# Kernel tuning notes

Measured on AMD Instinct MI355X. Metric: run time of the kernel, lower is better.

Reference implementation:

```python
import jax, jax.numpy as jnp
import numpy as np

B, T, I, H, L, O = 2048, 512, 1, 64, 2, 1


def _lstm_layer(x, Wih, Whh, b):
    """Single LSTM layer, batch_first x: [B, T, in] -> [B, T, H].
    PyTorch gate order: i, f, g, o. b = b_ih + b_hh (folded)."""
    Bn = x.shape[0]
    Hn = Whh.shape[1]
    # Precompute input contribution for all timesteps (hoisted out of scan)
    xg = jnp.einsum('bti,gi->btg', x, Wih) + b  # [B, T, 4H]

    def step(carry, xg_t):
        h, c = carry
        g = xg_t + h @ Whh.T  # [B, 4H]
        i, f, gg, o = jnp.split(g, 4, axis=-1)
        i = jax.nn.sigmoid(i)
        f = jax.nn.sigmoid(f)
        gg = jnp.tanh(gg)
        o = jax.nn.sigmoid(o)
        c = f * c + i * gg
        h = o * jnp.tanh(c)
        return (h, c), h

    h0 = jnp.zeros((Bn, Hn), x.dtype)
    c0 = jnp.zeros((Bn, Hn), x.dtype)
    (_, _), hs = jax.lax.scan(step, (h0, c0), jnp.swapaxes(xg, 0, 1))  # hs: [T, B, H]
    return jnp.swapaxes(hs, 0, 1)


def setup_inputs() -> dict:
    key = jax.random.key(0)
    ks = jax.random.split(key, 11)
    s = 1.0 / np.sqrt(H)  # torch default uniform bound
    u = lambda k, shp: jax.random.uniform(k, shp, jnp.float32, -s, s)
    return {
        'x': jax.random.normal(ks[0], (B, T, I), jnp.float32),
        'Wih0': u(ks[1], (4 * H, I)),
        'Whh0': u(ks[2], (4 * H, H)),
        'bih0': u(ks[3], (4 * H,)),
        'bhh0': u(ks[4], (4 * H,)),
        'Wih1': u(ks[5], (4 * H, H)),
        'Whh1': u(ks[6], (4 * H, H)),
        'bih1': u(ks[7], (4 * H,)),
        'bhh1': u(ks[8], (4 * H,)),
        'fcW': u(ks[9], (O, H)),
        'fcb': u(ks[10], (O,)),
    }


def reference(x, Wih0, Whh0, bih0, bhh0, Wih1, Whh1, bih1, bhh1, fcW, fcb):
    h1 = _lstm_layer(x, Wih0, Whh0, bih0 + bhh0)   # [B, T, H]
    h2 = _lstm_layer(h1, Wih1, Whh1, bih1 + bhh1)  # [B, T, H]
    return h2[:, -1, :] @ fcW.T + fcb               # [B, O]
```

## Files before the change

### kernel.cpp

```cpp
#include <hip/hip_runtime.h>


#define TT 512
#define HH 64
#define BT 8

typedef __attribute__((ext_vector_type(8))) short short8;
typedef __attribute__((ext_vector_type(4))) float f32x4;

#define MFMA16 __builtin_amdgcn_mfma_f32_16x16x32_bf16

__device__ __forceinline__ float sigm(float x) {
    return __builtin_amdgcn_rcpf(1.f + __expf(-x));
}
__device__ __forceinline__ float tanh_f(float x) {
    return 1.f - 2.f * __builtin_amdgcn_rcpf(1.f + __expf(2.f * x));
}
__device__ __forceinline__ void cvt8(const float* p, short8& hi, short8& lo) {
    #pragma unroll
    for (int i = 0; i < 8; ++i) {
        float v = p[i];
        unsigned short h = (unsigned short)(__float_as_uint(v) >> 16);
        float r = v - __uint_as_float(((unsigned)h) << 16);
        unsigned short l = (unsigned short)(__float_as_uint(r) >> 16);
        hi[i] = (short)h;
        lo[i] = (short)l;
    }
}
__device__ __forceinline__ void split1(float v, unsigned short& h, unsigned short& l) {
    h = (unsigned short)(__float_as_uint(v) >> 16);
    float r = v - __uint_as_float(((unsigned)h) << 16);
    l = (unsigned short)(__float_as_uint(r) >> 16);
}
__device__ __forceinline__ float gate4(float pi, float pf, float pg, float po, float& c) {
    float gi = sigm(pi), gf = sigm(pf), gg = tanh_f(pg), go = sigm(po);
    c = fmaf(gf, c, gi * gg);
    return go * tanh_f(c);
}
__device__ __forceinline__ float dpp_ror8(float v) {
    return __int_as_float(__builtin_amdgcn_update_dpp(
        0, __float_as_int(v), 0x128, 0xF, 0xF, true));
}

__global__ __launch_bounds__(1024) void lstm_mfma(
    const float* __restrict__ x,
    const float* __restrict__ Wih0, const float* __restrict__ Whh0,
    const float* __restrict__ bih0, const float* __restrict__ bhh0,
    const float* __restrict__ Wih1, const float* __restrict__ Whh1,
    const float* __restrict__ bih1, const float* __restrict__ bhh1,
    const float* __restrict__ fcW, const float* __restrict__ fcb,
    float* __restrict__ out)
{
    __shared__ float xs[BT][TT + 1];
    __shared__ __align__(16) short aH1[2][2][2][64][8];
    __shared__ __align__(16) short aH2[2][2][2][64][8];
    __shared__ float hF[BT][HH + 1];
    __shared__ float fcw_s[HH];

    const int t    = threadIdx.x;
    const int lane = t & 63;
    const int w    = t >> 6;
    const bool isL1 = (w < 8);
    const int wv   = w & 7;
    const int b0   = blockIdx.x * BT;
    const int m    = lane & 15;
    const int q    = lane >> 4;

    for (int i = t; i < BT * TT; i += 1024)
        xs[i >> 9][i & (TT - 1)] = x[(size_t)(b0 + (i >> 9)) * TT + (i & (TT - 1))];
    {
        int* z1 = (int*)aH1;
        for (int i = t; i < 2048; i += 1024) z1[i] = 0;
        int* z2 = (int*)aH2;
        for (int i = t; i < 2048; i += 1024) z2[i] = 0;
    }
    if (t < HH) fcw_s[t] = fcW[t];

    short8 aWh[2][4], aWl[2][4];
    {
        const float* Ws01 = isL1 ? Whh0 : Wih1;
        #pragma unroll
        for (int i = 0; i < 2; ++i) {
            const int mtg = 2 * wv + i;
            const int rho = (m & 3) * 64 + 4 * mtg + (m >> 2);
            cvt8(Ws01 + rho * HH +      q * 8, aWh[i][0], aWl[i][0]);
            cvt8(Ws01 + rho * HH + 32 + q * 8, aWh[i][1], aWl[i][1]);
            if (!isL1) {
                cvt8(Whh1 + rho * HH +      q * 8, aWh[i][2], aWl[i][2]);
                cvt8(Whh1 + rho * HH + 32 + q * 8, aWh[i][3], aWl[i][3]);
            }
        }
    }

    f32x4 biasD[2];
    #pragma unroll
    for (int i = 0; i < 2; ++i)
        #pragma unroll
        for (int r = 0; r < 4; ++r) {
            const int rho = r * 64 + 4 * (2 * wv + i) + q;
            biasD[i][r] = isL1 ? (bih0[rho] + bhh0[rho])
                               : (bih1[rho] + bhh1[rho]);
        }

    const int ts  = (m >> 3) & 1;
    const int jpk = 8 * wv + 4 * ts + q;
    const int bpk = m & 7;
    float wxb[4];
    #pragma unroll
    for (int v = 0; v < 4; ++v)
        wxb[v] = isL1 ? Wih0[v * 64 + jpk] : 0.f;
    const int skt = jpk >> 5;
    const int ssl = bpk + 16 * ((jpk >> 3) & 3);
    const int sse = jpk & 7;
    float c = 0.f;

    __syncthreads();

    #pragma unroll 2
    for (int k = 0; k < TT; ++k) {
        const int p = k & 1, pn = p ^ 1;

        if (isL1) {
            short8 bh0 = *(const short8*)&aH1[p][0][0][lane][0];
            short8 bl0 = *(const short8*)&aH1[p][0][1][lane][0];
            short8 bh1 = *(const short8*)&aH1[p][1][0][lane][0];
            short8 bl1 = *(const short8*)&aH1[p][1][1][lane][0];
            f32x4 acc0 = biasD[0], acc1 = biasD[1];
            acc0 = MFMA16(aWh[0][0], bh0, acc0, 0, 0, 0);
            acc1 = MFMA16(aWh[1][0], bh0, acc1, 0, 0, 0);
            acc0 = MFMA16(aWl[0][0], bh0, acc0, 0, 0, 0);
            acc1 = MFMA16(aWl[1][0], bh0, acc1, 0, 0, 0);
            acc0 = MFMA16(aWh[0][0], bl0, acc0, 0, 0, 0);
            acc1 = MFMA16(aWh[1][0], bl0, acc1, 0, 0, 0);
            acc0 = MFMA16(aWh[0][1], bh1, acc0, 0, 0, 0);
            acc1 = MFMA16(aWh[1][1], bh1, acc1, 0, 0, 0);
            acc0 = MFMA16(aWl[0][1], bh1, acc0, 0, 0, 0);
            acc1 = MFMA16(aWl[1][1], bh1, acc1, 0, 0, 0);
            acc0 = MFMA16(aWh[0][1], bl1, acc0, 0, 0, 0);
            acc1 = MFMA16(aWh[1][1], bl1, acc1, 0, 0, 0);
            f32x4 mv, pk;
            #pragma unroll
            for (int r = 0; r < 4; ++r) mv[r] = dpp_ror8(acc1[r]);
            #pragma unroll
            for (int r = 0; r < 4; ++r) pk[r] = (m < 8) ? acc0[r] : mv[r];
            float xb = xs[bpk][k];
            float h1 = gate4(fmaf(wxb[0], xb, pk[0]),
                             fmaf(wxb[1], xb, pk[1]),
                             fmaf(wxb[2], xb, pk[2]),
                             fmaf(wxb[3], xb, pk[3]), c);
            unsigned short hh, hl;
            split1(h1, hh, hl);
            aH1[pn][skt][0][ssl][sse] = (short)hh;
            aH1[pn][skt][1][ssl][sse] = (short)hl;
        } else if (k > 0) {
            short8 b1h0 = *(const short8*)&aH1[p][0][0][lane][0];
            short8 b1l0 = *(const short8*)&aH1[p][0][1][lane][0];
            short8 b1h1 = *(const short8*)&aH1[p][1][0][lane][0];
            short8 b1l1 = *(const short8*)&aH1[p][1][1][lane][0];
            short8 b2h0 = *(const short8*)&aH2[p][0][0][lane][0];
            short8 b2l0 = *(const short8*)&aH2[p][0][1][lane][0];
            short8 b2h1 = *(const short8*)&aH2[p][1][0][lane][0];
            short8 b2l1 = *(const short8*)&aH2[p][1][1][lane][0];
            f32x4 acc0 = biasD[0], acc1 = biasD[1];
            acc0 = MFMA16(aWh[0][0], b1h0, acc0, 0, 0, 0);
            acc1 = MFMA16(aWh[1][0], b1h0, acc1, 0, 0, 0);
            acc0 = MFMA16(aWl[0][0], b1h0, acc0, 0, 0, 0);
            acc1 = MFMA16(aWl[1][0], b1h0, acc1, 0, 0, 0);
            acc0 = MFMA16(aWh[0][0], b1l0, acc0, 0, 0, 0);
            acc1 = MFMA16(aWh[1][0], b1l0, acc1, 0, 0, 0);
            acc0 = MFMA16(aWh[0][1], b1h1, acc0, 0, 0, 0);
            acc1 = MFMA16(aWh[1][1], b1h1, acc1, 0, 0, 0);
            acc0 = MFMA16(aWl[0][1], b1h1, acc0, 0, 0, 0);
            acc1 = MFMA16(aWl[1][1], b1h1, acc1, 0, 0, 0);
            acc0 = MFMA16(aWh[0][1], b1l1, acc0, 0, 0, 0);
            acc1 = MFMA16(aWh[1][1], b1l1, acc1, 0, 0, 0);
            acc0 = MFMA16(aWh[0][2], b2h0, acc0, 0, 0, 0);
            acc1 = MFMA16(aWh[1][2], b2h0, acc1, 0, 0, 0);
            acc0 = MFMA16(aWl[0][2], b2h0, acc0, 0, 0, 0);
            acc1 = MFMA16(aWl[1][2], b2h0, acc1, 0, 0, 0);
            acc0 = MFMA16(aWh[0][2], b2l0, acc0, 0, 0, 0);
            acc1 = MFMA16(aWh[1][2], b2l0, acc1, 0, 0, 0);
            acc0 = MFMA16(aWh[0][3], b2h1, acc0, 0, 0, 0);
            acc1 = MFMA16(aWh[1][3], b2h1, acc1, 0, 0, 0);
            acc0 = MFMA16(aWl[0][3], b2h1, acc0, 0, 0, 0);
            acc1 = MFMA16(aWl[1][3], b2h1, acc1, 0, 0, 0);
            acc0 = MFMA16(aWh[0][3], b2l1, acc0, 0, 0, 0);
            acc1 = MFMA16(aWh[1][3], b2l1, acc1, 0, 0, 0);
            f32x4 mv, pk;
            #pragma unroll
            for (int r = 0; r < 4; ++r) mv[r] = dpp_ror8(acc1[r]);
            #pragma unroll
            for (int r = 0; r < 4; ++r) pk[r] = (m < 8) ? acc0[r] : mv[r];
            float h2 = gate4(pk[0], pk[1], pk[2], pk[3], c);
            unsigned short hh, hl;
            split1(h2, hh, hl);
            aH2[pn][skt][0][ssl][sse] = (short)hh;
            aH2[pn][skt][1][ssl][sse] = (short)hl;
        }
        __syncthreads();
    }

    if (!isL1) {
        short8 b1h0 = *(const short8*)&aH1[0][0][0][lane][0];
        short8 b1l0 = *(const short8*)&aH1[0][0][1][lane][0];
        short8 b1h1 = *(const short8*)&aH1[0][1][0][lane][0];
        short8 b1l1 = *(const short8*)&aH1[0][1][1][lane][0];
        short8 b2h0 = *(const short8*)&aH2[0][0][0][lane][0];
        short8 b2l0 = *(const short8*)&aH2[0][0][1][lane][0];
        short8 b2h1 = *(const short8*)&aH2[0][1][0][lane][0];
        short8 b2l1 = *(const short8*)&aH2[0][1][1][lane][0];
        f32x4 acc0 = biasD[0], acc1 = biasD[1];
        acc0 = MFMA16(aWh[0][0], b1h0, acc0, 0, 0, 0);
        acc1 = MFMA16(aWh[1][0], b1h0, acc1, 0, 0, 0);
        acc0 = MFMA16(aWl[0][0], b1h0, acc0, 0, 0, 0);
        acc1 = MFMA16(aWl[1][0], b1h0, acc1, 0, 0, 0);
        acc0 = MFMA16(aWh[0][0], b1l0, acc0, 0, 0, 0);
        acc1 = MFMA16(aWh[1][0], b1l0, acc1, 0, 0, 0);
        acc0 = MFMA16(aWh[0][1], b1h1, acc0, 0, 0, 0);
        acc1 = MFMA16(aWh[1][1], b1h1, acc1, 0, 0, 0);
        acc0 = MFMA16(aWl[0][1], b1h1, acc0, 0, 0, 0);
        acc1 = MFMA16(aWl[1][1], b1h1, acc1, 0, 0, 0);
        acc0 = MFMA16(aWh[0][1], b1l1, acc0, 0, 0, 0);
        acc1 = MFMA16(aWh[1][1], b1l1, acc1, 0, 0, 0);
        acc0 = MFMA16(aWh[0][2], b2h0, acc0, 0, 0, 0);
        acc1 = MFMA16(aWh[1][2], b2h0, acc1, 0, 0, 0);
        acc0 = MFMA16(aWl[0][2], b2h0, acc0, 0, 0, 0);
        acc1 = MFMA16(aWl[1][2], b2h0, acc1, 0, 0, 0);
        acc0 = MFMA16(aWh[0][2], b2l0, acc0, 0, 0, 0);
        acc1 = MFMA16(aWh[1][2], b2l0, acc1, 0, 0, 0);
        acc0 = MFMA16(aWh[0][3], b2h1, acc0, 0, 0, 0);
        acc1 = MFMA16(aWh[1][3], b2h1, acc1, 0, 0, 0);
        acc0 = MFMA16(aWl[0][3], b2h1, acc0, 0, 0, 0);
        acc1 = MFMA16(aWl[1][3], b2h1, acc1, 0, 0, 0);
        acc0 = MFMA16(aWh[0][3], b2l1, acc0, 0, 0, 0);
        acc1 = MFMA16(aWh[1][3], b2l1, acc1, 0, 0, 0);
        f32x4 mv, pk;
        #pragma unroll
        for (int r = 0; r < 4; ++r) mv[r] = dpp_ror8(acc1[r]);
        #pragma unroll
        for (int r = 0; r < 4; ++r) pk[r] = (m < 8) ? acc0[r] : mv[r];
        float h2 = gate4(pk[0], pk[1], pk[2], pk[3], c);
        hF[bpk][jpk] = h2;
    }
    __syncthreads();

    if (t < BT) {
        float s = fcb[0];
        #pragma unroll 8
        for (int j = 0; j < HH; ++j)
            s = fmaf(hF[t][j], fcw_s[j], s);
        out[b0 + t] = s;
    }
}

extern "C" void kernel_launch(void* const* d_in, const int* in_sizes, int n_in,
                              void* d_out, int out_size, void* d_ws, size_t ws_size,
                              hipStream_t stream) {
    const float* x    = (const float*)d_in[0];
    const float* Wih0 = (const float*)d_in[1];
    const float* Whh0 = (const float*)d_in[2];
    const float* bih0 = (const float*)d_in[3];
    const float* bhh0 = (const float*)d_in[4];
    const float* Wih1 = (const float*)d_in[5];
    const float* Whh1 = (const float*)d_in[6];
    const float* bih1 = (const float*)d_in[7];
    const float* bhh1 = (const float*)d_in[8];
    const float* fcW  = (const float*)d_in[9];
    const float* fcb  = (const float*)d_in[10];
    float* out = (float*)d_out;

    lstm_mfma<<<dim3(2048 / BT), dim3(1024), 0, stream>>>(
        x, Wih0, Whh0, bih0, bhh0, Wih1, Whh1, bih1, bhh1, fcW, fcb, out);
}
```

Baseline: 505.5 us.

## Pack hi/lo hidden splits into one MFMA B operand and fold via DPP

The hidden-state bf16 hi and lo parts are now stored in the same 16-column MFMA B tile (lo in columns 8-15), so each K chunk needs one B load instead of two. Each weight-split product (Wh·[hh|hl], Wl·[hh|hl]) then covers both halves at once, cutting layer-1 MFMAs from 12 to 8 and layer-2 from 24 to 16. Partial sums are folded across the column halves with a DPP rotate-by-8 add, and the bias is halved to compensate for being added twice. The cost is extra DPP adds and a small extra Wl·hl term, traded against fewer MFMAs and LDS reads on the serial recurrence path.

New measurement: 512.5 us. No clear change (+1.4%).

```diff
diff --git a/kernel.cpp b/kernel.cpp
--- a/kernel.cpp
+++ b/kernel.cpp
@@ -52,8 +52,8 @@
     float* __restrict__ out)
 {
     __shared__ float xs[BT][TT + 1];
-    __shared__ __align__(16) short aH1[2][2][2][64][8];
-    __shared__ __align__(16) short aH2[2][2][2][64][8];
+    __shared__ __align__(16) short aH1[2][2][64][8];
+    __shared__ __align__(16) short aH2[2][2][64][8];
     __shared__ float hF[BT][HH + 1];
     __shared__ float fcw_s[HH];
 
@@ -70,9 +70,9 @@
         xs[i >> 9][i & (TT - 1)] = x[(size_t)(b0 + (i >> 9)) * TT + (i & (TT - 1))];
     {
         int* z1 = (int*)aH1;
-        for (int i = t; i < 2048; i += 1024) z1[i] = 0;
+        if (t < 1024) z1[t] = 0;
         int* z2 = (int*)aH2;
-        for (int i = t; i < 2048; i += 1024) z2[i] = 0;
+        if (t < 1024) z2[t] = 0;
     }
     if (t < HH) fcw_s[t] = fcW[t];
 
@@ -98,8 +98,8 @@
         #pragma unroll
         for (int r = 0; r < 4; ++r) {
             const int rho = r * 64 + 4 * (2 * wv + i) + q;
-            biasD[i][r] = isL1 ? (bih0[rho] + bhh0[rho])
-                               : (bih1[rho] + bhh1[rho]);
+            biasD[i][r] = 0.5f * (isL1 ? (bih0[rho] + bhh0[rho])
+                                       : (bih1[rho] + bhh1[rho]));
         }
 
     const int ts  = (m >> 3) & 1;
@@ -121,28 +121,24 @@
         const int p = k & 1, pn = p ^ 1;
 
         if (isL1) {
-            short8 bh0 = *(const short8*)&aH1[p][0][0][lane][0];
-            short8 bl0 = *(const short8*)&aH1[p][0][1][lane][0];
-            short8 bh1 = *(const short8*)&aH1[p][1][0][lane][0];
-            short8 bl1 = *(const short8*)&aH1[p][1][1][lane][0];
+            short8 B0 = *(const short8*)&aH1[p][0][lane][0];
+            short8 B1 = *(const short8*)&aH1[p][1][lane][0];
             f32x4 acc0 = biasD[0], acc1 = biasD[1];
-            acc0 = MFMA16(aWh[0][0], bh0, acc0, 0, 0, 0);
-            acc1 = MFMA16(aWh[1][0], bh0, acc1, 0, 0, 0);
-            acc0 = MFMA16(aWl[0][0], bh0, acc0, 0, 0, 0);
-            acc1 = MFMA16(aWl[1][0], bh0, acc1, 0, 0, 0);
-            acc0 = MFMA16(aWh[0][0], bl0, acc0, 0, 0, 0);
-            acc1 = MFMA16(aWh[1][0], bl0, acc1, 0, 0, 0);
-            acc0 = MFMA16(aWh[0][1], bh1, acc0, 0, 0, 0);
-            acc1 = MFMA16(aWh[1][1], bh1, acc1, 0, 0, 0);
-            acc0 = MFMA16(aWl[0][1], bh1, acc0, 0, 0, 0);
-            acc1 = MFMA16(aWl[1][1], bh1, acc1, 0, 0, 0);
-            acc0 = MFMA16(aWh[0][1], bl1, acc0, 0, 0, 0);
-            acc1 = MFMA16(aWh[1][1], bl1, acc1, 0, 0, 0);
-            f32x4 mv, pk;
-            #pragma unroll
-            for (int r = 0; r < 4; ++r) mv[r] = dpp_ror8(acc1[r]);
-            #pragma unroll
-            for (int r = 0; r < 4; ++r) pk[r] = (m < 8) ? acc0[r] : mv[r];
+            acc0 = MFMA16(aWh[0][0], B0, acc0, 0, 0, 0);
+            acc1 = MFMA16(aWh[1][0], B0, acc1, 0, 0, 0);
+            acc0 = MFMA16(aWl[0][0], B0, acc0, 0, 0, 0);
+            acc1 = MFMA16(aWl[1][0], B0, acc1, 0, 0, 0);
+            acc0 = MFMA16(aWh[0][1], B1, acc0, 0, 0, 0);
+            acc1 = MFMA16(aWh[1][1], B1, acc1, 0, 0, 0);
+            acc0 = MFMA16(aWl[0][1], B1, acc0, 0, 0, 0);
+            acc1 = MFMA16(aWl[1][1], B1, acc1, 0, 0, 0);
+            f32x4 s0, s1, pk;
+            #pragma unroll
+            for (int r = 0; r < 4; ++r) s0[r] = acc0[r] + dpp_ror8(acc0[r]);
+            #pragma unroll
+            for (int r = 0; r < 4; ++r) s1[r] = acc1[r] + dpp_ror8(acc1[r]);
+            #pragma unroll
+            for (int r = 0; r < 4; ++r) pk[r] = (m < 8) ? s0[r] : s1[r];
             float xb = xs[bpk][k];
             float h1 = gate4(fmaf(wxb[0], xb, pk[0]),
                              fmaf(wxb[1], xb, pk[1]),
@@ -150,95 +146,75 @@
                              fmaf(wxb[3], xb, pk[3]), c);
             unsigned short hh, hl;
             split1(h1, hh, hl);
-            aH1[pn][skt][0][ssl][sse] = (short)hh;
-            aH1[pn][skt][1][ssl][sse] = (short)hl;
+            aH1[pn][skt][ssl][sse]     = (short)hh;
+            aH1[pn][skt][ssl + 8][sse] = (short)hl;
         } else if (k > 0) {
-            short8 b1h0 = *(const short8*)&aH1[p][0][0][lane][0];
-            short8 b1l0 = *(const short8*)&aH1[p][0][1][lane][0];
-            short8 b1h1 = *(const short8*)&aH1[p][1][0][lane][0];
-            short8 b1l1 = *(const short8*)&aH1[p][1][1][lane][0];
-            short8 b2h0 = *(const short8*)&aH2[p][0][0][lane][0];
-            short8 b2l0 = *(const short8*)&aH2[p][0][1][lane][0];
-            short8 b2h1 = *(const short8*)&aH2[p][1][0][lane][0];
-            short8 b2l1 = *(const short8*)&aH2[p][1][1][lane][0];
+            short8 B10 = *(const short8*)&aH1[p][0][lane][0];
+            short8 B11 = *(const short8*)&aH1[p][1][lane][0];
+            short8 B20 = *(const short8*)&aH2[p][0][lane][0];
+            short8 B21 = *(const short8*)&aH2[p][1][lane][0];
             f32x4 acc0 = biasD[0], acc1 = biasD[1];
-            acc0 = MFMA16(aWh[0][0], b1h0, acc0, 0, 0, 0);
-            acc1 = MFMA16(aWh[1][0], b1h0, acc1, 0, 0, 0);
-            acc0 = MFMA16(aWl[0][0], b1h0, acc0, 0, 0, 0);
-            acc1 = MFMA16(aWl[1][0], b1h0, acc1, 0, 0, 0);
-            acc0 = MFMA16(aWh[0][0], b1l0, acc0, 0, 0, 0);
-            acc1 = MFMA16(aWh[1][0], b1l0, acc1, 0, 0, 0);
-            acc0 = MFMA16(aWh[0][1], b1h1, acc0, 0, 0, 0);
-            acc1 = MFMA16(aWh[1][1], b1h1, acc1, 0, 0, 0);
-            acc0 = MFMA16(aWl[0][1], b1h1, acc0, 0, 0, 0);
-            acc1 = MFMA16(aWl[1][1], b1h1, acc1, 0, 0, 0);
-            acc0 = MFMA16(aWh[0][1], b1l1, acc0, 0, 0, 0);
-            acc1 = MFMA16(aWh[1][1], b1l1, acc1, 0, 0, 0);
-            acc0 = MFMA16(aWh[0][2], b2h0, acc0, 0, 0, 0);
-            acc1 = MFMA16(aWh[1][2], b2h0, acc1, 0, 0, 0);
-            acc0 = MFMA16(aWl[0][2], b2h0, acc0, 0, 0, 0);
-            acc1 = MFMA16(aWl[1][2], b2h0, acc1, 0, 0, 0);
-            acc0 = MFMA16(aWh[0][2], b2l0, acc0, 0, 0, 0);
-            acc1 = MFMA16(aWh[1][2], b2l0, acc1, 0, 0, 0);
-            acc0 = MFMA16(aWh[0][3], b2h1, acc0, 0, 0, 0);
-            acc1 = MFMA16(aWh[1][3], b2h1, acc1, 0, 0, 0);
-            acc0 = MFMA16(aWl[0][3], b2h1, acc0, 0, 0, 0);
-            acc1 = MFMA16(aWl[1][3], b2h1, acc1, 0, 0, 0);
-            acc0 = MFMA16(aWh[0][3], b2l1, acc0, 0, 0, 0);
-            acc1 = MFMA16(aWh[1][3], b2l1, acc1, 0, 0, 0);
-            f32x4 mv, pk;
-            #pragma unroll
-            for (int r = 0; r < 4; ++r) mv[r] = dpp_ror8(acc1[r]);
-            #pragma unroll
-            for (int r = 0; r < 4; ++r) pk[r] = (m < 8) ? acc0[r] : mv[r];
+            acc0 = MFMA16(aWh[0][0], B10, acc0, 0, 0, 0);
+            acc1 = MFMA16(aWh[1][0], B10, acc1, 0, 0, 0);
+            acc0 = MFMA16(aWl[0][0], B10, acc0, 0, 0, 0);
+            acc1 = MFMA16(aWl[1][0], B10, acc1, 0, 0, 0);
+            acc0 = MFMA16(aWh[0][1], B11, acc0, 0, 0, 0);
+            acc1 = MFMA16(aWh[1][1], B11, acc1, 0, 0, 0);
+            acc0 = MFMA16(aWl[0][1], B11, acc0, 0, 0, 0);
+            acc1 = MFMA16(aWl[1][1], B11, acc1, 0, 0, 0);
+            acc0 = MFMA16(aWh[0][2], B20, acc0, 0, 0, 0);
+            acc1 = MFMA16(aWh[1][2], B20, acc1, 0, 0, 0);
+            acc0 = MFMA16(aWl[0][2], B20, acc0, 0, 0, 0);
+            acc1 = MFMA16(aWl[1][2], B20, acc1, 0, 0, 0);
+            acc0 = MFMA16(aWh[0][3], B21, acc0, 0, 0, 0);
+            acc1 = MFMA16(aWh[1][3], B21, acc1, 0, 0, 0);
+            acc0 = MFMA16(aWl[0][3], B21, acc0, 0, 0, 0);
+            acc1 = MFMA16(aWl[1][3], B21, acc1, 0, 0, 0);
+            f32x4 s0, s1, pk;
+            #pragma unroll
+            for (int r = 0; r < 4; ++r) s0[r] = acc0[r] + dpp_ror8(acc0[r]);
+            #pragma unroll
+            for (int r = 0; r < 4; ++r) s1[r] = acc1[r] + dpp_ror8(acc1[r]);
+            #pragma unroll
+            for (int r = 0; r < 4; ++r) pk[r] = (m < 8) ? s0[r] : s1[r];
             float h2 = gate4(pk[0], pk[1], pk[2], pk[3], c);
             unsigned short hh, hl;
             split1(h2, hh, hl);
-            aH2[pn][skt][0][ssl][sse] = (short)hh;
-            aH2[pn][skt][1][ssl][sse] = (short)hl;
+            aH2[pn][skt][ssl][sse]     = (short)hh;
+            aH2[pn][skt][ssl + 8][sse] = (short)hl;
         }
         __syncthreads();
     }
 
     if (!isL1) {
-        short8 b1h0 = *(const short8*)&aH1[0][0][0][lane][0];
-        short8 b1l0 = *(const short8*)&aH1[0][0][1][lane][0];
-        short8 b1h1 = *(const short8*)&aH1[0][1][0][lane][0];
-        short8 b1l1 = *(const short8*)&aH1[0][1][1][lane][0];
-        short8 b2h0 = *(const short8*)&aH2[0][0][0][lane][0];
-        short8 b2l0 = *(const short8*)&aH2[0][0][1][lane][0];
-        short8 b2h1 = *(const short8*)&aH2[0][1][0][lane][0];
-        short8 b2l1 = *(const short8*)&aH2[0][1][1][lane][0];
+        short8 B10 = *(const short8*)&aH1[0][0][lane][0];
+        short8 B11 = *(const short8*)&aH1[0][1][lane][0];
+        short8 B20 = *(const short8*)&aH2[0][0][lane][0];
+        short8 B21 = *(const short8*)&aH2[0][1][lane][0];
         f32x4 acc0 = biasD[0], acc1 = biasD[1];
-        acc0 = MFMA16(aWh[0][0], b1h0, acc0, 0, 0, 0);
-        acc1 = MFMA16(aWh[1][0], b1h0, acc1, 0, 0, 0);
-        acc0 = MFMA16(aWl[0][0], b1h0, acc0, 0, 0, 0);
-        acc1 = MFMA16(aWl[1][0], b1h0, acc1, 0, 0, 0);
-        acc0 = MFMA16(aWh[0][0], b1l0, acc0, 0, 0, 0);
-        acc1 = MFMA16(aWh[1][0], b1l0, acc1, 0, 0, 0);
-        acc0 = MFMA16(aWh[0][1], b1h1, acc0, 0, 0, 0);
-        acc1 = MFMA16(aWh[1][1], b1h1, acc1, 0, 0, 0);
-        acc0 = MFMA16(aWl[0][1], b1h1, acc0, 0, 0, 0);
-        acc1 = MFMA16(aWl[1][1], b1h1, acc1, 0, 0, 0);
-        acc0 = MFMA16(aWh[0][1], b1l1, acc0, 0, 0, 0);
-        acc1 = MFMA16(aWh[1][1], b1l1, acc1, 0, 0, 0);
-        acc0 = MFMA16(aWh[0][2], b2h0, acc0, 0, 0, 0);
-        acc1 = MFMA16(aWh[1][2], b2h0, acc1, 0, 0, 0);
-        acc0 = MFMA16(aWl[0][2], b2h0, acc0, 0, 0, 0);
-        acc1 = MFMA16(aWl[1][2], b2h0, acc1, 0, 0, 0);
-        acc0 = MFMA16(aWh[0][2], b2l0, acc0, 0, 0, 0);
-        acc1 = MFMA16(aWh[1][2], b2l0, acc1, 0, 0, 0);
-        acc0 = MFMA16(aWh[0][3], b2h1, acc0, 0, 0, 0);
-        acc1 = MFMA16(aWh[1][3], b2h1, acc1, 0, 0, 0);
-        acc0 = MFMA16(aWl[0][3], b2h1, acc0, 0, 0, 0);
-        acc1 = MFMA16(aWl[1][3], b2h1, acc1, 0, 0, 0);
-        acc0 = MFMA16(aWh[0][3], b2l1, acc0, 0, 0, 0);
-        acc1 = MFMA16(aWh[1][3], b2l1, acc1, 0, 0, 0);
-        f32x4 mv, pk;
-        #pragma unroll
-        for (int r = 0; r < 4; ++r) mv[r] = dpp_ror8(acc1[r]);
-        #pragma unroll
-        for (int r = 0; r < 4; ++r) pk[r] = (m < 8) ? acc0[r] : mv[r];
+        acc0 = MFMA16(aWh[0][0], B10, acc0, 0, 0, 0);
+        acc1 = MFMA16(aWh[1][0], B10, acc1, 0, 0, 0);
+        acc0 = MFMA16(aWl[0][0], B10, acc0, 0, 0, 0);
+        acc1 = MFMA16(aWl[1][0], B10, acc1, 0, 0, 0);
+        acc0 = MFMA16(aWh[0][1], B11, acc0, 0, 0, 0);
+        acc1 = MFMA16(aWh[1][1], B11, acc1, 0, 0, 0);
+        acc0 = MFMA16(aWl[0][1], B11, acc0, 0, 0, 0);
+        acc1 = MFMA16(aWl[1][1], B11, acc1, 0, 0, 0);
+        acc0 = MFMA16(aWh[0][2], B20, acc0, 0, 0, 0);
+        acc1 = MFMA16(aWh[1][2], B20, acc1, 0, 0, 0);
+        acc0 = MFMA16(aWl[0][2], B20, acc0, 0, 0, 0);
+        acc1 = MFMA16(aWl[1][2], B20, acc1, 0, 0, 0);
+        acc0 = MFMA16(aWh[0][3], B21, acc0, 0, 0, 0);
+        acc1 = MFMA16(aWh[1][3], B21, acc1, 0, 0, 0);
+        acc0 = MFMA16(aWl[0][3], B21, acc0, 0, 0, 0);
+        acc1 = MFMA16(aWl[1][3], B21, acc1, 0, 0, 0);
+        f32x4 s0, s1, pk;
+        #pragma unroll
+        for (int r = 0; r < 4; ++r) s0[r] = acc0[r] + dpp_ror8(acc0[r]);
+        #pragma unroll
+        for (int r = 0; r < 4; ++r) s1[r] = acc1[r] + dpp_ror8(acc1[r]);
+        #pragma unroll
+        for (int r = 0; r < 4; ++r) pk[r] = (m < 8) ? s0[r] : s1[r];
         float h2 = gate4(pk[0], pk[1], pk[2], pk[3], c);
         hF[bpk][jpk] = h2;
     }
```
